# Kernel tuning notes

Hardware: AMD Instinct MI355X
Metric: run time of the kernel (lower is better)

The kernel has to match this reference:

```python
import jax, jax.numpy as jnp
import numpy as np

N_NODES = 100000
N_EDGES = 1200000
D_FEAT = 64


def setup_inputs() -> dict:
    key = jax.random.key(0)
    k1, k2, k3 = jax.random.split(key, 3)
    u_f = jax.random.normal(k1, (N_NODES, D_FEAT), dtype=jnp.float32)
    src = jax.random.randint(k2, (N_EDGES,), 0, N_NODES, dtype=jnp.int32)
    dst = jax.random.randint(k3, (N_EDGES,), 0, N_NODES, dtype=jnp.int32)
    return {"u_f": u_f, "src": src, "dst": dst}


def reference(u_f, src, dst):
    n = u_f.shape[0]
    ones = jnp.ones(src.shape[0], dtype=u_f.dtype)
    # out-degree normalization (messages flow src -> dst)
    out_deg = jnp.clip(jax.ops.segment_sum(ones, src, num_segments=n), 1.0)
    node_f = u_f * (out_deg ** -0.5)[:, None]
    # copy_u + sum aggregation: gather src features, scatter-add onto dst
    rst = jax.ops.segment_sum(node_f[src], dst, num_segments=n)
    in_deg = jnp.clip(jax.ops.segment_sum(ones, dst, num_segments=n), 1.0)
    rst = rst * (in_deg ** -0.5)[:, None]
    return rst
```

## Files before the change

kernel.cpp:

```cpp
#include <hip/hip_runtime.h>
#include <hip/hip_fp16.h>

#define D_FEAT 64
#define BUCKET_BITS 7
#define BUCKET_NODES (1 << BUCKET_BITS)
#define HALF_NODES 64
#define BIN_TILE 4096
#define SRC_BITS 17
#define SRC_MASK ((1u << SRC_BITS) - 1u)
#define HIST_BLOCKS 240
#define NBP 800
#define CAP2 2048

__global__ void k_hist(const int* __restrict__ src, const int* __restrict__ dst,
                       int* __restrict__ hist_part, int n_edges) {
    __shared__ int hs[NBP], hd[NBP];
    const int t = threadIdx.x;
    for (int i = t; i < NBP; i += 256) { hs[i] = 0; hd[i] = 0; }
    __syncthreads();
    const int4* s4 = reinterpret_cast<const int4*>(src);
    const int4* d4 = reinterpret_cast<const int4*>(dst);
    const int n4 = n_edges >> 2;
    for (int i = blockIdx.x * blockDim.x + t; i < n4; i += gridDim.x * blockDim.x) {
        int4 a = s4[i], b = d4[i];
        atomicAdd(&hs[a.x >> BUCKET_BITS], 1); atomicAdd(&hs[a.y >> BUCKET_BITS], 1);
        atomicAdd(&hs[a.z >> BUCKET_BITS], 1); atomicAdd(&hs[a.w >> BUCKET_BITS], 1);
        atomicAdd(&hd[b.x >> BUCKET_BITS], 1); atomicAdd(&hd[b.y >> BUCKET_BITS], 1);
        atomicAdd(&hd[b.z >> BUCKET_BITS], 1); atomicAdd(&hd[b.w >> BUCKET_BITS], 1);
    }
    const int rem = n_edges & 3;
    if (blockIdx.x == 0 && t < rem) {
        int e = (n_edges & ~3) + t;
        atomicAdd(&hs[src[e] >> BUCKET_BITS], 1);
        atomicAdd(&hd[dst[e] >> BUCKET_BITS], 1);
    }
    __syncthreads();
    int* outp = hist_part + (size_t)blockIdx.x * 2 * NBP;
    for (int i = t; i < NBP; i += 256) { outp[i] = hs[i]; outp[NBP + i] = hd[i]; }
}

__global__ void k_reduce(const int* __restrict__ hist_part, int* __restrict__ btot_s,
                         int* __restrict__ btot_d, int n_buckets) {
    const int j = (blockIdx.x * blockDim.x + threadIdx.x) >> 6;
    const int lane = threadIdx.x & 63;
    if (j >= 2 * n_buckets) return;
    const int which = (j >= n_buckets) ? 1 : 0;
    const int b = j - which * n_buckets;
    int v = 0;
    for (int i = lane; i < HIST_BLOCKS; i += 64)
        v += hist_part[((size_t)i * 2 + which) * NBP + b];
    #pragma unroll
    for (int off = 32; off; off >>= 1) v += __shfl_down(v, off);
    if (lane == 0) { if (which) btot_d[b] = v; else btot_s[b] = v; }
}

__global__ void __launch_bounds__(1024)
k_scan(const int* __restrict__ btot_s, const int* __restrict__ btot_d,
       int* __restrict__ boff_s, int* __restrict__ gcur_s,
       int* __restrict__ boff_d, int* __restrict__ gcur_d,
       int n_buckets, int n_edges) {
    __shared__ int sh[1024];
    const int t = threadIdx.x;
    int v = (t < n_buckets) ? btot_s[t] : 0;
    sh[t] = v; __syncthreads();
    for (int off = 1; off < 1024; off <<= 1) {
        int x = (t >= off) ? sh[t - off] : 0; __syncthreads();
        sh[t] += x; __syncthreads();
    }
    if (t < n_buckets) { boff_s[t] = sh[t] - v; gcur_s[t] = sh[t] - v; }
    if (t == 0) boff_s[n_buckets] = n_edges;
    __syncthreads();
    int w = (t < n_buckets) ? btot_d[t] : 0;
    sh[t] = w; __syncthreads();
    for (int off = 1; off < 1024; off <<= 1) {
        int x = (t >= off) ? sh[t - off] : 0; __syncthreads();
        sh[t] += x; __syncthreads();
    }
    if (t < n_buckets) { boff_d[t] = sh[t] - w; gcur_d[t] = sh[t] - w; }
    if (t == 0) boff_d[n_buckets] = n_edges;
}

__global__ void __launch_bounds__(1024)
k_bin12(const int* __restrict__ src, const int* __restrict__ dst,
        int* __restrict__ gcur_s, int* __restrict__ gcur_d,
        unsigned char* __restrict__ u8, unsigned* __restrict__ packed,
        int n_edges, int n_buckets) {
    __shared__ int hs[1024], hd[1024];
    __shared__ int delta_s[1024], delta_d[1024];
    __shared__ unsigned valw[BIN_TILE];
    __shared__ unsigned short bb_s[BIN_TILE], bb_d[BIN_TILE];
    __shared__ unsigned char val8[BIN_TILE];

    const int t = threadIdx.x;
    const int base = blockIdx.x * BIN_TILE;
    const int tcount = min(BIN_TILE, n_edges - base);
    hs[t] = 0; hd[t] = 0;
    __syncthreads();

    int es[4], ed[4];
    const int e0 = base + (t << 2);
    if (e0 + 3 < n_edges) {
        int4 a = *reinterpret_cast<const int4*>(src + e0);
        int4 b = *reinterpret_cast<const int4*>(dst + e0);
        es[0] = a.x; es[1] = a.y; es[2] = a.z; es[3] = a.w;
        ed[0] = b.x; ed[1] = b.y; ed[2] = b.z; ed[3] = b.w;
    } else {
        #pragma unroll
        for (int j = 0; j < 4; ++j) {
            if (e0 + j < n_edges) { es[j] = src[e0 + j]; ed[j] = dst[e0 + j]; }
            else { es[j] = -1; ed[j] = 0; }
        }
    }
    #pragma unroll
    for (int j = 0; j < 4; ++j) if (es[j] >= 0) {
        atomicAdd(&hs[es[j] >> BUCKET_BITS], 1);
        atomicAdd(&hd[ed[j] >> BUCKET_BITS], 1);
    }
    __syncthreads();

    const int cs = hs[t], cd = hd[t];
    const int p = cs | (cd << 16);
    hs[t] = p;
    __syncthreads();
    for (int off = 1; off < 1024; off <<= 1) {
        int x = (t >= off) ? hs[t - off] : 0; __syncthreads();
        hs[t] += x; __syncthreads();
    }
    const int excl = hs[t] - p;
    const int excl_s = excl & 0xFFFF;
    const int excl_d = (excl >> 16) & 0xFFFF;
    __syncthreads();
    hs[t] = excl_s; hd[t] = excl_d;
    if (t < n_buckets) {
        if (cs > 0) delta_s[t] = atomicAdd(&gcur_s[t], cs) - excl_s;
        if (cd > 0) delta_d[t] = atomicAdd(&gcur_d[t], cd) - excl_d;
    }
    __syncthreads();

    #pragma unroll
    for (int j = 0; j < 4; ++j) if (es[j] >= 0) {
        const int b1 = es[j] >> BUCKET_BITS;
        const int p1 = atomicAdd(&hs[b1], 1);
        val8[p1] = (unsigned char)(es[j] & (BUCKET_NODES - 1));
        bb_s[p1] = (unsigned short)b1;
        const int b2 = ed[j] >> BUCKET_BITS;
        const int p2 = atomicAdd(&hd[b2], 1);
        valw[p2] = ((unsigned)(ed[j] & (BUCKET_NODES - 1)) << SRC_BITS) | (unsigned)es[j];
        bb_d[p2] = (unsigned short)b2;
    }
    __syncthreads();

    for (int i = t; i < tcount; i += 1024) {
        u8[i + delta_s[bb_s[i]]] = val8[i];
        packed[i + delta_d[bb_d[i]]] = valw[i];
    }
}

__global__ void __launch_bounds__(256)
k_cnt_prescale(const unsigned char* __restrict__ u8, const int* __restrict__ boff_s,
               const float* __restrict__ u_f, unsigned short* __restrict__ nf,
               int n_nodes) {
    __shared__ int scnt[BUCKET_NODES];
    __shared__ float osc[BUCKET_NODES];
    const int t = threadIdx.x, b = blockIdx.x;
    const int lo = boff_s[b], hi = boff_s[b + 1];
    if (t < BUCKET_NODES) scnt[t] = 0;
    __syncthreads();
    for (int i = lo + t; i < hi; i += 256) atomicAdd(&scnt[u8[i]], 1);
    __syncthreads();
    if (t < BUCKET_NODES) osc[t] = rsqrtf((float)max(scnt[t], 1));
    __syncthreads();
    const int node0 = b << BUCKET_BITS;
    const int nn = min(BUCKET_NODES, n_nodes - node0);
    const float4* uf4 = reinterpret_cast<const float4*>(u_f + ((size_t)node0 << 6));
    uint2* nf2 = reinterpret_cast<uint2*>(nf + ((size_t)node0 << 6));
    for (int i = t; i < nn * 16; i += 256) {
        const float w = osc[i >> 4];
        float4 v = uf4[i];
        uint2 p;
        p.x = (unsigned)__half_as_ushort(__float2half_rn(v.x * w)) |
              ((unsigned)__half_as_ushort(__float2half_rn(v.y * w)) << 16);
        p.y = (unsigned)__half_as_ushort(__float2half_rn(v.z * w)) |
              ((unsigned)__half_as_ushort(__float2half_rn(v.w * w)) << 16);
        nf2[i] = p;
    }
}

__device__ inline void acc8(float* a, uint4 q) {
    union { unsigned u; __half2 h; } c;
    float2 f;
    c.u = q.x; f = __half22float2(c.h); a[0] += f.x; a[1] += f.y;
    c.u = q.y; f = __half22float2(c.h); a[2] += f.x; a[3] += f.y;
    c.u = q.z; f = __half22float2(c.h); a[4] += f.x; a[5] += f.y;
    c.u = q.w; f = __half22float2(c.h); a[6] += f.x; a[7] += f.y;
}

__global__ void __launch_bounds__(256)
k_agg2(const unsigned* __restrict__ packed, const int* __restrict__ boff_d,
       const unsigned short* __restrict__ nf, float* __restrict__ out,
       int n_nodes) {
    __shared__ int scnt[HALF_NODES];
    __shared__ int sstart[HALF_NODES];
    __shared__ int scur[HALF_NODES];
    __shared__ int nperm[HALF_NODES];
    __shared__ int dh[64];
    __shared__ int stot;
    __shared__ int lsrc[CAP2];

    const int t = threadIdx.x;
    const int b = blockIdx.x >> 1;
    const int h = blockIdx.x & 1;
    const int lo = boff_d[b], hi = boff_d[b + 1];
    const int ne = hi - lo;
    const int nodeBase = (b << BUCKET_BITS) + h * HALF_NODES;
    const int g2 = t >> 3, o = t & 7;

    if (t < HALF_NODES) scnt[t] = 0;
    if (t < 64) dh[t] = 0;
    __syncthreads();

    for (int i = t; i < ne; i += 256) {
        const unsigned p = packed[lo + i];
        const int dl = (int)(p >> SRC_BITS);
        if ((dl >> 6) == h) atomicAdd(&scnt[dl & 63], 1);
    }
    __syncthreads();

    if (t < 64) {
        const int v = scnt[t];
        atomicAdd(&dh[min(v, 63)], 1);
        int s = v;
        #pragma unroll
        for (int off = 1; off < 64; off <<= 1) {
            int x = __shfl_up(s, off);
            if (t >= off) s += x;
        }
        sstart[t] = s - v;
        scur[t] = s - v;
        if (t == 63) stot = s;
    }
    __syncthreads();
    if (t < 64) {
        const int v = dh[t];
        int s = v;
        #pragma unroll
        for (int off = 1; off < 64; off <<= 1) {
            int x = __shfl_up(s, off);
            if (t >= off) s += x;
        }
        dh[t] = s - v;
    }
    __syncthreads();
    if (t < HALF_NODES) {
        const int pos = atomicAdd(&dh[min(scnt[t], 63)], 1);
        nperm[pos] = t;
    }
    __syncthreads();

    if (stot <= CAP2) {
        for (int i = t; i < ne; i += 256) {
            const unsigned p = packed[lo + i];
            const int dl = (int)(p >> SRC_BITS);
            if ((dl >> 6) == h) {
                const int pos = atomicAdd(&scur[dl & 63], 1);
                lsrc[pos] = (int)(p & SRC_MASK);
            }
        }
        __syncthreads();

        #pragma unroll
        for (int it = 0; it < HALF_NODES / 32; ++it) {
            const int nl = nperm[it * 32 + g2];
            const int node = nodeBase + nl;
            if (node >= n_nodes) continue;
            const int start = sstart[nl];
            const int cnt = scnt[nl];
            const unsigned short* base = nf + o * 8;
            float acc[8] = {0.f,0.f,0.f,0.f,0.f,0.f,0.f,0.f};
            int k = 0;
            for (; k + 8 <= cnt; k += 8) {
                int s0 = lsrc[start+k+0], s1 = lsrc[start+k+1];
                int s2 = lsrc[start+k+2], s3 = lsrc[start+k+3];
                int s4 = lsrc[start+k+4], s5 = lsrc[start+k+5];
                int s6 = lsrc[start+k+6], s7 = lsrc[start+k+7];
                uint4 q0 = *reinterpret_cast<const uint4*>(base + ((size_t)s0 << 6));
                uint4 q1 = *reinterpret_cast<const uint4*>(base + ((size_t)s1 << 6));
                uint4 q2 = *reinterpret_cast<const uint4*>(base + ((size_t)s2 << 6));
                uint4 q3 = *reinterpret_cast<const uint4*>(base + ((size_t)s3 << 6));
                uint4 q4 = *reinterpret_cast<const uint4*>(base + ((size_t)s4 << 6));
                uint4 q5 = *reinterpret_cast<const uint4*>(base + ((size_t)s5 << 6));
                uint4 q6 = *reinterpret_cast<const uint4*>(base + ((size_t)s6 << 6));
                uint4 q7 = *reinterpret_cast<const uint4*>(base + ((size_t)s7 << 6));
                acc8(acc, q0); acc8(acc, q1); acc8(acc, q2); acc8(acc, q3);
                acc8(acc, q4); acc8(acc, q5); acc8(acc, q6); acc8(acc, q7);
            }
            for (; k + 4 <= cnt; k += 4) {
                int s0 = lsrc[start+k+0], s1 = lsrc[start+k+1];
                int s2 = lsrc[start+k+2], s3 = lsrc[start+k+3];
                uint4 q0 = *reinterpret_cast<const uint4*>(base + ((size_t)s0 << 6));
                uint4 q1 = *reinterpret_cast<const uint4*>(base + ((size_t)s1 << 6));
                uint4 q2 = *reinterpret_cast<const uint4*>(base + ((size_t)s2 << 6));
                uint4 q3 = *reinterpret_cast<const uint4*>(base + ((size_t)s3 << 6));
                acc8(acc, q0); acc8(acc, q1); acc8(acc, q2); acc8(acc, q3);
            }
            for (; k < cnt; ++k) {
                int s = lsrc[start + k];
                uint4 q = *reinterpret_cast<const uint4*>(base + ((size_t)s << 6));
                acc8(acc, q);
            }
            const float isc = rsqrtf((float)max(cnt, 1));
            float4 r0 = make_float4(acc[0]*isc, acc[1]*isc, acc[2]*isc, acc[3]*isc);
            float4 r1 = make_float4(acc[4]*isc, acc[5]*isc, acc[6]*isc, acc[7]*isc);
            float4* orow = reinterpret_cast<float4*>(out + ((size_t)node << 6) + o * 8);
            orow[0] = r0;
            orow[1] = r1;
        }
    } else {
        for (int it = 0; it < HALF_NODES / 32; ++it) {
            const int nl = it * 32 + g2;
            const int node = nodeBase + nl;
            if (node >= n_nodes) continue;
            const unsigned short* base = nf + o * 8;
            float acc[8] = {0.f,0.f,0.f,0.f,0.f,0.f,0.f,0.f};
            int cnt = 0;
            for (int i = 0; i < ne; ++i) {
                const unsigned p = packed[lo + i];
                if ((int)(p >> SRC_BITS) == (h << 6) + nl) {
                    const int s = (int)(p & SRC_MASK);
                    uint4 q = *reinterpret_cast<const uint4*>(base + ((size_t)s << 6));
                    acc8(acc, q);
                    ++cnt;
                }
            }
            const float isc = rsqrtf((float)max(cnt, 1));
            float4 r0 = make_float4(acc[0]*isc, acc[1]*isc, acc[2]*isc, acc[3]*isc);
            float4 r1 = make_float4(acc[4]*isc, acc[5]*isc, acc[6]*isc, acc[7]*isc);
            float4* orow = reinterpret_cast<float4*>(out + ((size_t)node << 6) + o * 8);
            orow[0] = r0;
            orow[1] = r1;
        }
    }
}

extern "C" void kernel_launch(void* const* d_in, const int* in_sizes, int n_in,
                              void* d_out, int out_size, void* d_ws, size_t ws_size,
                              hipStream_t stream) {
    const float* u_f = (const float*)d_in[0];
    const int*   src = (const int*)d_in[1];
    const int*   dst = (const int*)d_in[2];
    float* out = (float*)d_out;

    const int n_nodes = in_sizes[0] / D_FEAT;
    const int n_edges = in_sizes[1];
    const int n_buckets = (n_nodes + BUCKET_NODES - 1) >> BUCKET_BITS;

    int* w = (int*)d_ws;
    size_t off = 0;
    auto alloc = [&](size_t nwords) { int* p = w + off; off += (nwords + 3) & ~(size_t)3; return p; };
    int* btot_s   = alloc(n_buckets);
    int* btot_d   = alloc(n_buckets);
    int* boff_s   = alloc(n_buckets + 1);
    int* boff_d   = alloc(n_buckets + 1);
    int* gcur_s   = alloc(n_buckets);
    int* gcur_d   = alloc(n_buckets);
    size_t hist_words = (size_t)HIST_BLOCKS * 2 * NBP;
    size_t u8_words = ((size_t)n_edges + 3) >> 2;
    size_t regA_words = hist_words > u8_words ? hist_words : u8_words;
    int* regionA  = alloc(regA_words);
    unsigned* packed = (unsigned*)alloc(n_edges);
    unsigned short* nf16 = (unsigned short*)alloc((size_t)n_nodes * (D_FEAT / 2));

    int* hist_part    = regionA;
    unsigned char* u8 = (unsigned char*)regionA;

    const int bin_blocks = (n_edges + BIN_TILE - 1) / BIN_TILE;
    const int red_blocks = (2 * n_buckets * 64 + 255) / 256;

    k_hist<<<HIST_BLOCKS, 256, 0, stream>>>(src, dst, hist_part, n_edges);
    k_reduce<<<red_blocks, 256, 0, stream>>>(hist_part, btot_s, btot_d, n_buckets);
    k_scan<<<1, 1024, 0, stream>>>(btot_s, btot_d, boff_s, gcur_s, boff_d, gcur_d,
                                   n_buckets, n_edges);
    k_bin12<<<bin_blocks, 1024, 0, stream>>>(src, dst, gcur_s, gcur_d, u8, packed,
                                             n_edges, n_buckets);
    k_cnt_prescale<<<n_buckets, 256, 0, stream>>>(u8, boff_s, u_f, nf16, n_nodes);
    k_agg2<<<n_buckets * 2, 256, 0, stream>>>(packed, boff_d, nf16, out, n_nodes);
}
```

Before: 78.15 us.

## Fuse reduce+scan into one kernel, use wave scans, split aggregation into quarter buckets

Merges the histogram reduction and the bucket scan into a single-block kernel, which removes one launch. Block-wide shared-memory scans in the scan and binning kernels are replaced with wave-level shuffle scans plus a small cross-wave pass. The aggregation kernel now gives 4 blocks per bucket of 32 nodes each, up from 2 blocks of 64. It also preloads each bucket's packed edges into registers once, instead of reading them from global memory twice. The cost is that the single-block reduction reads 240 partial histograms serially, and quartering the bucket means each block re-reads the same packed edges.

```diff
diff --git a/kernel.cpp b/kernel.cpp
--- a/kernel.cpp
+++ b/kernel.cpp
@@ -4,13 +4,23 @@
 #define D_FEAT 64
 #define BUCKET_BITS 7
 #define BUCKET_NODES (1 << BUCKET_BITS)
-#define HALF_NODES 64
+#define QN 32
 #define BIN_TILE 4096
 #define SRC_BITS 17
 #define SRC_MASK ((1u << SRC_BITS) - 1u)
 #define HIST_BLOCKS 240
 #define NBP 800
-#define CAP2 2048
+#define CAP1 1024
+#define PBUF 12
+
+__device__ __forceinline__ int wave_incl_scan64(int v, int lane) {
+    #pragma unroll
+    for (int off = 1; off < 64; off <<= 1) {
+        int x = __shfl_up(v, off);
+        if (lane >= off) v += x;
+    }
+    return v;
+}
 
 __global__ void k_hist(const int* __restrict__ src, const int* __restrict__ dst,
                        int* __restrict__ hist_part, int n_edges) {
@@ -39,45 +49,48 @@
     for (int i = t; i < NBP; i += 256) { outp[i] = hs[i]; outp[NBP + i] = hd[i]; }
 }
 
-__global__ void k_reduce(const int* __restrict__ hist_part, int* __restrict__ btot_s,
-                         int* __restrict__ btot_d, int n_buckets) {
-    const int j = (blockIdx.x * blockDim.x + threadIdx.x) >> 6;
-    const int lane = threadIdx.x & 63;
-    if (j >= 2 * n_buckets) return;
-    const int which = (j >= n_buckets) ? 1 : 0;
-    const int b = j - which * n_buckets;
-    int v = 0;
-    for (int i = lane; i < HIST_BLOCKS; i += 64)
-        v += hist_part[((size_t)i * 2 + which) * NBP + b];
-    #pragma unroll
-    for (int off = 32; off; off >>= 1) v += __shfl_down(v, off);
-    if (lane == 0) { if (which) btot_d[b] = v; else btot_s[b] = v; }
-}
-
 __global__ void __launch_bounds__(1024)
-k_scan(const int* __restrict__ btot_s, const int* __restrict__ btot_d,
-       int* __restrict__ boff_s, int* __restrict__ gcur_s,
-       int* __restrict__ boff_d, int* __restrict__ gcur_d,
-       int n_buckets, int n_edges) {
-    __shared__ int sh[1024];
-    const int t = threadIdx.x;
-    int v = (t < n_buckets) ? btot_s[t] : 0;
-    sh[t] = v; __syncthreads();
-    for (int off = 1; off < 1024; off <<= 1) {
-        int x = (t >= off) ? sh[t - off] : 0; __syncthreads();
-        sh[t] += x; __syncthreads();
-    }
-    if (t < n_buckets) { boff_s[t] = sh[t] - v; gcur_s[t] = sh[t] - v; }
-    if (t == 0) boff_s[n_buckets] = n_edges;
-    __syncthreads();
-    int w = (t < n_buckets) ? btot_d[t] : 0;
-    sh[t] = w; __syncthreads();
-    for (int off = 1; off < 1024; off <<= 1) {
-        int x = (t >= off) ? sh[t - off] : 0; __syncthreads();
-        sh[t] += x; __syncthreads();
-    }
-    if (t < n_buckets) { boff_d[t] = sh[t] - w; gcur_d[t] = sh[t] - w; }
-    if (t == 0) boff_d[n_buckets] = n_edges;
+k_rscan(const int* __restrict__ hist_part,
+        int* __restrict__ boff_s, int* __restrict__ gcur_s,
+        int* __restrict__ boff_d, int* __restrict__ gcur_d,
+        int n_buckets, int n_edges) {
+    __shared__ int ws1[16], ws2[16];
+    const int t = threadIdx.x, lane = t & 63, wid = t >> 6;
+    int vs = 0, vd = 0;
+    if (t < n_buckets) {
+        #pragma unroll 4
+        for (int i = 0; i < HIST_BLOCKS; ++i) {
+            vs += hist_part[(size_t)i * 2 * NBP + t];
+            vd += hist_part[(size_t)i * 2 * NBP + NBP + t];
+        }
+    }
+    int incl = wave_incl_scan64(vs, lane);
+    if (lane == 63) ws1[wid] = incl;
+    __syncthreads();
+    if (wid == 0) {
+        int w = (lane < 16) ? ws1[lane] : 0;
+        #pragma unroll
+        for (int off = 1; off < 16; off <<= 1) { int x = __shfl_up(w, off); if (lane >= off) w += x; }
+        if (lane < 16) ws1[lane] = w;
+    }
+    __syncthreads();
+    const int excl_s = ((wid > 0) ? ws1[wid - 1] : 0) + incl - vs;
+    int incl2 = wave_incl_scan64(vd, lane);
+    if (lane == 63) ws2[wid] = incl2;
+    __syncthreads();
+    if (wid == 0) {
+        int w = (lane < 16) ? ws2[lane] : 0;
+        #pragma unroll
+        for (int off = 1; off < 16; off <<= 1) { int x = __shfl_up(w, off); if (lane >= off) w += x; }
+        if (lane < 16) ws2[lane] = w;
+    }
+    __syncthreads();
+    const int excl_d = ((wid > 0) ? ws2[wid - 1] : 0) + incl2 - vd;
+    if (t < n_buckets) {
+        boff_s[t] = excl_s; gcur_s[t] = excl_s;
+        boff_d[t] = excl_d; gcur_d[t] = excl_d;
+    }
+    if (t == 0) { boff_s[n_buckets] = n_edges; boff_d[n_buckets] = n_edges; }
 }
 
 __global__ void __launch_bounds__(1024)
@@ -87,11 +100,13 @@
         int n_edges, int n_buckets) {
     __shared__ int hs[1024], hd[1024];
     __shared__ int delta_s[1024], delta_d[1024];
+    __shared__ int wsum[16];
     __shared__ unsigned valw[BIN_TILE];
     __shared__ unsigned short bb_s[BIN_TILE], bb_d[BIN_TILE];
     __shared__ unsigned char val8[BIN_TILE];
 
     const int t = threadIdx.x;
+    const int lane = t & 63, wid = t >> 6;
     const int base = blockIdx.x * BIN_TILE;
     const int tcount = min(BIN_TILE, n_edges - base);
     hs[t] = 0; hd[t] = 0;
@@ -119,17 +134,20 @@
     __syncthreads();
 
     const int cs = hs[t], cd = hd[t];
-    const int p = cs | (cd << 16);
-    hs[t] = p;
-    __syncthreads();
-    for (int off = 1; off < 1024; off <<= 1) {
-        int x = (t >= off) ? hs[t - off] : 0; __syncthreads();
-        hs[t] += x; __syncthreads();
-    }
-    const int excl = hs[t] - p;
+    const int pv = cs | (cd << 16);
+    int incl = wave_incl_scan64(pv, lane);
+    if (lane == 63) wsum[wid] = incl;
+    __syncthreads();
+    if (wid == 0) {
+        int w = (lane < 16) ? wsum[lane] : 0;
+        #pragma unroll
+        for (int off = 1; off < 16; off <<= 1) { int x = __shfl_up(w, off); if (lane >= off) w += x; }
+        if (lane < 16) wsum[lane] = w;
+    }
+    __syncthreads();
+    const int excl = ((wid > 0) ? wsum[wid - 1] : 0) + incl - pv;
     const int excl_s = excl & 0xFFFF;
     const int excl_d = (excl >> 16) & 0xFFFF;
-    __syncthreads();
     hs[t] = excl_s; hd[t] = excl_d;
     if (t < n_buckets) {
         if (cs > 0) delta_s[t] = atomicAdd(&gcur_s[t], cs) - excl_s;
@@ -196,48 +214,56 @@
 }
 
 __global__ void __launch_bounds__(256)
-k_agg2(const unsigned* __restrict__ packed, const int* __restrict__ boff_d,
+k_agg4(const unsigned* __restrict__ packed, const int* __restrict__ boff_d,
        const unsigned short* __restrict__ nf, float* __restrict__ out,
        int n_nodes) {
-    __shared__ int scnt[HALF_NODES];
-    __shared__ int sstart[HALF_NODES];
-    __shared__ int scur[HALF_NODES];
-    __shared__ int nperm[HALF_NODES];
+    __shared__ int scnt[QN], sstart[QN], scur[QN], nperm[QN];
     __shared__ int dh[64];
-    __shared__ int stot;
-    __shared__ int lsrc[CAP2];
+    __shared__ int lsrc[CAP1];
 
     const int t = threadIdx.x;
-    const int b = blockIdx.x >> 1;
-    const int h = blockIdx.x & 1;
+    const int b = blockIdx.x >> 2;
+    const int h = blockIdx.x & 3;
     const int lo = boff_d[b], hi = boff_d[b + 1];
     const int ne = hi - lo;
-    const int nodeBase = (b << BUCKET_BITS) + h * HALF_NODES;
+    const int nodeBase = (b << BUCKET_BITS) + h * QN;
     const int g2 = t >> 3, o = t & 7;
-
-    if (t < HALF_NODES) scnt[t] = 0;
+    const bool big = ne > PBUF * 256;
+
+    unsigned pbuf[PBUF];
+    if (!big) {
+        #pragma unroll
+        for (int j = 0; j < PBUF; ++j) {
+            const int i = j * 256 + t;
+            pbuf[j] = (i < ne) ? packed[lo + i] : 0xFFFFFFFFu;
+        }
+    }
+
+    if (t < QN) scnt[t] = 0;
     if (t < 64) dh[t] = 0;
     __syncthreads();
 
-    for (int i = t; i < ne; i += 256) {
-        const unsigned p = packed[lo + i];
-        const int dl = (int)(p >> SRC_BITS);
-        if ((dl >> 6) == h) atomicAdd(&scnt[dl & 63], 1);
-    }
-    __syncthreads();
-
+    if (!big) {
+        #pragma unroll
+        for (int j = 0; j < PBUF; ++j) {
+            const int dl = (int)(pbuf[j] >> SRC_BITS);
+            if ((dl >> 5) == h) atomicAdd(&scnt[dl & 31], 1);
+        }
+    }
+    __syncthreads();
+
+    __shared__ int stot_sh;
     if (t < 64) {
-        const int v = scnt[t];
-        atomicAdd(&dh[min(v, 63)], 1);
+        const int v = (t < QN) ? scnt[t] : 0;
+        if (t < QN) atomicAdd(&dh[min(v, 63)], 1);
         int s = v;
         #pragma unroll
         for (int off = 1; off < 64; off <<= 1) {
             int x = __shfl_up(s, off);
             if (t >= off) s += x;
         }
-        sstart[t] = s - v;
-        scur[t] = s - v;
-        if (t == 63) stot = s;
+        if (t < QN) { sstart[t] = s - v; scur[t] = s - v; }
+        if (t == QN - 1) stot_sh = s;
     }
     __syncthreads();
     if (t < 64) {
@@ -251,94 +277,90 @@
         dh[t] = s - v;
     }
     __syncthreads();
-    if (t < HALF_NODES) {
+    if (t < QN) {
         const int pos = atomicAdd(&dh[min(scnt[t], 63)], 1);
         nperm[pos] = t;
     }
     __syncthreads();
 
-    if (stot <= CAP2) {
-        for (int i = t; i < ne; i += 256) {
+    const bool fast = !big && (stot_sh <= CAP1);
+    if (fast) {
+        #pragma unroll
+        for (int j = 0; j < PBUF; ++j) {
+            const int dl = (int)(pbuf[j] >> SRC_BITS);
+            if ((dl >> 5) == h) {
+                const int pos = atomicAdd(&scur[dl & 31], 1);
+                lsrc[pos] = (int)(pbuf[j] & SRC_MASK);
+            }
+        }
+        __syncthreads();
+
+        const int nl = nperm[g2];
+        const int node = nodeBase + nl;
+        if (node >= n_nodes) return;
+        const int start = sstart[nl];
+        const int cnt = scnt[nl];
+        const unsigned short* base = nf + o * 8;
+        float acc[8] = {0.f,0.f,0.f,0.f,0.f,0.f,0.f,0.f};
+        int k = 0;
+        for (; k + 8 <= cnt; k += 8) {
+            int s0 = lsrc[start+k+0], s1 = lsrc[start+k+1];
+            int s2 = lsrc[start+k+2], s3 = lsrc[start+k+3];
+            int s4 = lsrc[start+k+4], s5 = lsrc[start+k+5];
+            int s6 = lsrc[start+k+6], s7 = lsrc[start+k+7];
+            uint4 q0 = *reinterpret_cast<const uint4*>(base + ((size_t)s0 << 6));
+            uint4 q1 = *reinterpret_cast<const uint4*>(base + ((size_t)s1 << 6));
+            uint4 q2 = *reinterpret_cast<const uint4*>(base + ((size_t)s2 << 6));
+            uint4 q3 = *reinterpret_cast<const uint4*>(base + ((size_t)s3 << 6));
+            uint4 q4 = *reinterpret_cast<const uint4*>(base + ((size_t)s4 << 6));
+            uint4 q5 = *reinterpret_cast<const uint4*>(base + ((size_t)s5 << 6));
+            uint4 q6 = *reinterpret_cast<const uint4*>(base + ((size_t)s6 << 6));
+            uint4 q7 = *reinterpret_cast<const uint4*>(base + ((size_t)s7 << 6));
+            acc8(acc, q0); acc8(acc, q1); acc8(acc, q2); acc8(acc, q3);
+            acc8(acc, q4); acc8(acc, q5); acc8(acc, q6); acc8(acc, q7);
+        }
+        for (; k + 4 <= cnt; k += 4) {
+            int s0 = lsrc[start+k+0], s1 = lsrc[start+k+1];
+            int s2 = lsrc[start+k+2], s3 = lsrc[start+k+3];
+            uint4 q0 = *reinterpret_cast<const uint4*>(base + ((size_t)s0 << 6));
+            uint4 q1 = *reinterpret_cast<const uint4*>(base + ((size_t)s1 << 6));
+            uint4 q2 = *reinterpret_cast<const uint4*>(base + ((size_t)s2 << 6));
+            uint4 q3 = *reinterpret_cast<const uint4*>(base + ((size_t)s3 << 6));
+            acc8(acc, q0); acc8(acc, q1); acc8(acc, q2); acc8(acc, q3);
+        }
+        for (; k < cnt; ++k) {
+            int s = lsrc[start + k];
+            uint4 q = *reinterpret_cast<const uint4*>(base + ((size_t)s << 6));
+            acc8(acc, q);
+        }
+        const float isc = rsqrtf((float)max(cnt, 1));
+        float4 r0 = make_float4(acc[0]*isc, acc[1]*isc, acc[2]*isc, acc[3]*isc);
+        float4 r1 = make_float4(acc[4]*isc, acc[5]*isc, acc[6]*isc, acc[7]*isc);
+        float4* orow = reinterpret_cast<float4*>(out + ((size_t)node << 6) + o * 8);
+        orow[0] = r0;
+        orow[1] = r1;
+    } else {
+        const int nl = g2;
+        const int node = nodeBase + nl;
+        if (node >= n_nodes) return;
+        const unsigned short* base = nf + o * 8;
+        float acc[8] = {0.f,0.f,0.f,0.f,0.f,0.f,0.f,0.f};
+        int cnt = 0;
+        for (int i = 0; i < ne; ++i) {
             const unsigned p = packed[lo + i];
-            const int dl = (int)(p >> SRC_BITS);
-            if ((dl >> 6) == h) {
-                const int pos = atomicAdd(&scur[dl & 63], 1);
-                lsrc[pos] = (int)(p & SRC_MASK);
-            }
-        }
-        __syncthreads();
-
-        #pragma unroll
-        for (int it = 0; it < HALF_NODES / 32; ++it) {
-            const int nl = nperm[it * 32 + g2];
-            const int node = nodeBase + nl;
-            if (node >= n_nodes) continue;
-            const int start = sstart[nl];
-            const int cnt = scnt[nl];
-            const unsigned short* base = nf + o * 8;
-            float acc[8] = {0.f,0.f,0.f,0.f,0.f,0.f,0.f,0.f};
-            int k = 0;
-            for (; k + 8 <= cnt; k += 8) {
-                int s0 = lsrc[start+k+0], s1 = lsrc[start+k+1];
-                int s2 = lsrc[start+k+2], s3 = lsrc[start+k+3];
-                int s4 = lsrc[start+k+4], s5 = lsrc[start+k+5];
-                int s6 = lsrc[start+k+6], s7 = lsrc[start+k+7];
-                uint4 q0 = *reinterpret_cast<const uint4*>(base + ((size_t)s0 << 6));
-                uint4 q1 = *reinterpret_cast<const uint4*>(base + ((size_t)s1 << 6));
-                uint4 q2 = *reinterpret_cast<const uint4*>(base + ((size_t)s2 << 6));
-                uint4 q3 = *reinterpret_cast<const uint4*>(base + ((size_t)s3 << 6));
-                uint4 q4 = *reinterpret_cast<const uint4*>(base + ((size_t)s4 << 6));
-                uint4 q5 = *reinterpret_cast<const uint4*>(base + ((size_t)s5 << 6));
-                uint4 q6 = *reinterpret_cast<const uint4*>(base + ((size_t)s6 << 6));
-                uint4 q7 = *reinterpret_cast<const uint4*>(base + ((size_t)s7 << 6));
-                acc8(acc, q0); acc8(acc, q1); acc8(acc, q2); acc8(acc, q3);
-                acc8(acc, q4); acc8(acc, q5); acc8(acc, q6); acc8(acc, q7);
-            }
-            for (; k + 4 <= cnt; k += 4) {
-                int s0 = lsrc[start+k+0], s1 = lsrc[start+k+1];
-                int s2 = lsrc[start+k+2], s3 = lsrc[start+k+3];
-                uint4 q0 = *reinterpret_cast<const uint4*>(base + ((size_t)s0 << 6));
-                uint4 q1 = *reinterpret_cast<const uint4*>(base + ((size_t)s1 << 6));
-                uint4 q2 = *reinterpret_cast<const uint4*>(base + ((size_t)s2 << 6));
-                uint4 q3 = *reinterpret_cast<const uint4*>(base + ((size_t)s3 << 6));
-                acc8(acc, q0); acc8(acc, q1); acc8(acc, q2); acc8(acc, q3);
-            }
-            for (; k < cnt; ++k) {
-                int s = lsrc[start + k];
+            if ((int)(p >> SRC_BITS) == (h << 5) + nl) {
+                const int s = (int)(p & SRC_MASK);
                 uint4 q = *reinterpret_cast<const uint4*>(base + ((size_t)s << 6));
                 acc8(acc, q);
+                ++cnt;
             }
-            const float isc = rsqrtf((float)max(cnt, 1));
-            float4 r0 = make_float4(acc[0]*isc, acc[1]*isc, acc[2]*isc, acc[3]*isc);
-            float4 r1 = make_float4(acc[4]*isc, acc[5]*isc, acc[6]*isc, acc[7]*isc);
-            float4* orow = reinterpret_cast<float4*>(out + ((size_t)node << 6) + o * 8);
-            orow[0] = r0;
-            orow[1] = r1;
-        }
-    } else {
-        for (int it = 0; it < HALF_NODES / 32; ++it) {
-            const int nl = it * 32 + g2;
-            const int node = nodeBase + nl;
-            if (node >= n_nodes) continue;
-            const unsigned short* base = nf + o * 8;
-            float acc[8] = {0.f,0.f,0.f,0.f,0.f,0.f,0.f,0.f};
-            int cnt = 0;
-            for (int i = 0; i < ne; ++i) {
-                const unsigned p = packed[lo + i];
-                if ((int)(p >> SRC_BITS) == (h << 6) + nl) {
-                    const int s = (int)(p & SRC_MASK);
-                    uint4 q = *reinterpret_cast<const uint4*>(base + ((size_t)s << 6));
-                    acc8(acc, q);
-                    ++cnt;
-                }
-            }
-            const float isc = rsqrtf((float)max(cnt, 1));
-            float4 r0 = make_float4(acc[0]*isc, acc[1]*isc, acc[2]*isc, acc[3]*isc);
-            float4 r1 = make_float4(acc[4]*isc, acc[5]*isc, acc[6]*isc, acc[7]*isc);
-            float4* orow = reinterpret_cast<float4*>(out + ((size_t)node << 6) + o * 8);
-            orow[0] = r0;
-            orow[1] = r1;
-        }
+        }
+        const float isc = rsqrtf((float)max(cnt, 1));
+        float4 r0 = make_float4(acc[0]*isc, acc[1]*isc, acc[2]*isc, acc[3]*isc);
+        float4 r1 = make_float4(acc[4]*isc, acc[5]*isc, acc[6]*isc, acc[7]*isc);
+        float4* orow = reinterpret_cast<float4*>(out + ((size_t)node << 6) + o * 8);
+        orow[0] = r0;
+        orow[1] = r1;
     }
 }
 
@@ -357,8 +379,6 @@
     int* w = (int*)d_ws;
     size_t off = 0;
     auto alloc = [&](size_t nwords) { int* p = w + off; off += (nwords + 3) & ~(size_t)3; return p; };
-    int* btot_s   = alloc(n_buckets);
-    int* btot_d   = alloc(n_buckets);
     int* boff_s   = alloc(n_buckets + 1);
     int* boff_d   = alloc(n_buckets + 1);
     int* gcur_s   = alloc(n_buckets);
@@ -374,14 +394,12 @@
     unsigned char* u8 = (unsigned char*)regionA;
 
     const int bin_blocks = (n_edges + BIN_TILE - 1) / BIN_TILE;
-    const int red_blocks = (2 * n_buckets * 64 + 255) / 256;
 
     k_hist<<<HIST_BLOCKS, 256, 0, stream>>>(src, dst, hist_part, n_edges);
-    k_reduce<<<red_blocks, 256, 0, stream>>>(hist_part, btot_s, btot_d, n_buckets);
-    k_scan<<<1, 1024, 0, stream>>>(btot_s, btot_d, boff_s, gcur_s, boff_d, gcur_d,
-                                   n_buckets, n_edges);
+    k_rscan<<<1, 1024, 0, stream>>>(hist_part, boff_s, gcur_s, boff_d, gcur_d,
+                                    n_buckets, n_edges);
     k_bin12<<<bin_blocks, 1024, 0, stream>>>(src, dst, gcur_s, gcur_d, u8, packed,
                                              n_edges, n_buckets);
     k_cnt_prescale<<<n_buckets, 256, 0, stream>>>(u8, boff_s, u_f, nf16, n_nodes);
-    k_agg2<<<n_buckets * 2, 256, 0, stream>>>(packed, boff_d, nf16, out, n_nodes);
-}
+    k_agg4<<<n_buckets * 4, 256, 0, stream>>>(packed, boff_d, nf16, out, n_nodes);
+}
```

Measured after the change: 85.67 us. 1.1x slower.
